# Kernel optimization log

Measured on AMD Instinct MI355X. Metric: run time of the kernel, lower is better.

The kernel has to match this reference:

```python
import jax, jax.numpy as jnp
import numpy as np

MODES = 16  # FourierLayer default


def _fourier_layer(h, w):
    # h: [B, S, H] real; w: [H, H, MODES] complex
    S = h.shape[1]
    h_ft = jnp.fft.rfft(h, axis=1)                 # [B, F, H] complex, F = S//2+1
    m = min(MODES, h_ft.shape[1])
    # batched complex matmul over the retained low-frequency modes
    out_m = jnp.einsum('bmh,hkm->bmk', h_ft[:, :m, :], w[:, :, :m])
    out_ft = jnp.zeros_like(h_ft).at[:, :m, :].set(out_m)  # higher modes zeroed
    h = jnp.fft.irfft(out_ft, n=S, axis=1)
    return jax.nn.gelu(h, approximate=False)       # torch nn.GELU() is exact erf


def setup_inputs() -> dict:
    key = jax.random.key(0)
    ks = jax.random.split(key, 7)
    B, S, H, L = 32, 8192, 128, 4
    x = jax.random.normal(ks[0], (B, S), jnp.float32)
    proj_w = jax.random.normal(ks[1], (H,), jnp.float32)          # Linear(1,H).weight[:,0]
    proj_b = jax.random.normal(ks[2], (H,), jnp.float32) * 0.02
    w_re = jax.random.normal(ks[3], (L, H, H, MODES), jnp.float32) * 0.02
    w_im = jax.random.normal(ks[4], (L, H, H, MODES), jnp.float32) * 0.02
    out_w = jax.random.normal(ks[5], (H,), jnp.float32) * 0.02    # Linear(H,1).weight[0]
    out_b = jax.random.normal(ks[6], (1,), jnp.float32) * 0.02
    return {"x": x, "proj_w": proj_w, "proj_b": proj_b,
            "w_re": w_re, "w_im": w_im, "out_w": out_w, "out_b": out_b}


def reference(x, proj_w, proj_b, w_re, w_im, out_w, out_b):
    # projection: Linear(1, H) applied to x.unsqueeze(-1)
    h = x[..., None] * proj_w + proj_b            # [B, S, H]
    W = (w_re + 1j * w_im).astype(jnp.complex64)  # [L, H, H, MODES]
    for l in range(w_re.shape[0]):                # fixed small layer count
        h = _fourier_layer(h, W[l])
    # output projection Linear(H, 1) then squeeze(-1)
    return h @ out_w + out_b[0]                   # [B, S]
```

## Files before the change

### kernel.cpp

```cpp
#include <hip/hip_runtime.h>
#include <hip/hip_bf16.h>

#define S_LEN 8192
#define NH 128
#define NM 16
#define NB 32
#define NBATCH 32
#define GP2 136

typedef __hip_bfloat16 bf16;
typedef unsigned short ushort_t;
typedef unsigned int uint_t;

typedef __bf16 bf16x8 __attribute__((ext_vector_type(8)));
typedef float floatx4 __attribute__((ext_vector_type(4)));

__device__ __forceinline__ float b2f(bf16 v){ return __bfloat162float(v); }
__device__ __forceinline__ float ldf(const void* p, long i, int f32){
    return f32 ? ((const float*)p)[i] : b2f(((const bf16*)p)[i]);
}
__device__ __forceinline__ float gelu_fast(float x){
    float z = fabsf(x) * 0.70710678118654752440f;
    float t = __builtin_amdgcn_rcpf(__builtin_fmaf(0.3275911f, z, 1.0f));
    float p = t*(0.254829592f + t*(-0.284496736f + t*(1.421413741f +
              t*(-1.453152027f + t*1.061405429f))));
    float e = __expf(-z * z);
    float er = __builtin_fmaf(-p, e, 1.0f);
    float s = copysignf(er, x);
    return 0.5f * x * (1.0f + s);
}
__device__ __forceinline__ ushort_t f2us(float v){
    return __builtin_bit_cast(ushort_t, (__bf16)v);
}
__device__ __forceinline__ void split_bf(float v, ushort_t& hi, ushort_t& lo){
    __bf16 h = (__bf16)v;
    float r = v - (float)h;
    hi = __builtin_bit_cast(ushort_t, h);
    lo = __builtin_bit_cast(ushort_t, (__bf16)r);
}
__device__ __forceinline__ bf16x8 ld8(const ushort_t* p){
    return *(const bf16x8*)(const void*)p;
}
__device__ __forceinline__ floatx4 MF(bf16x8 a, bf16x8 b, floatx4 c){
    return __builtin_amdgcn_mfma_f32_16x16x32_bf16(a, b, c, 0, 0, 0);
}

__device__ __forceinline__ int detect_f32(const void* x, int tid){
    __shared__ int sflag;
    if (tid < 64){
        const ushort_t* p = (const ushort_t*)x;
        int cnt = 0;
        for (int i = tid; i < 4096; i += 64){
            int e = (p[i] >> 7) & 0xFF;
            if (e >= 0xA0) cnt++;
        }
        #pragma unroll
        for (int off = 32; off > 0; off >>= 1) cnt += __shfl_xor(cnt, off, 64);
        if (tid == 0) sflag = (cnt > 400) ? 1 : 0;
    }
    __syncthreads();
    return sflag;
}

__device__ __forceinline__ void c_prologue(const float* __restrict__ C,
                                           int b, int c, int q,
                                           bf16x8* Bhi, bf16x8* Blo){
    const float* Cb = C + (long)b * NB * NH;
    #pragma unroll
    for (int kt = 0; kt < 8; kt++){
        int k = kt * 16 + c;
        bf16x8 h8, l8;
        #pragma unroll
        for (int e = 0; e < 8; e++){
            int j = 8 * q + e;
            float sc = (j == 0) ? (1.0f / S_LEN)
                     : (j < NM) ? (2.0f / S_LEN)
                     : (j == NM) ? 0.f : (-2.0f / S_LEN);
            float v = Cb[j * NH + k] * sc;
            __bf16 hh = (__bf16)v;
            h8[e] = hh;
            l8[e] = (__bf16)(v - (float)hh);
        }
        Bhi[kt] = h8; Blo[kt] = l8;
    }
}

__global__ __launch_bounds__(256) void k_prep(const void* __restrict__ x,
                                              const void* __restrict__ pw,
                                              const void* __restrict__ pb,
                                              float* __restrict__ M,
                                              ushort_t* __restrict__ Thi,
                                              ushort_t* __restrict__ Tlo,
                                              ushort_t* __restrict__ TThi,
                                              float* __restrict__ C0){
    int bid = blockIdx.x;
    int tid = threadIdx.x;
    int f32 = detect_f32(x, tid);
    if (bid < 512){
        int m = bid >> 5, b = bid & 31;
        float re = 0.f, im = 0.f;
        #pragma unroll 4
        for (int s = tid; s < S_LEN; s += 256){
            float xv = ldf(x, (long)b * S_LEN + s, f32);
            if (m){
                int r = (m * s) & (S_LEN - 1);
                float rev = (float)r * (1.0f / (float)S_LEN);
                float sv = __builtin_amdgcn_sinf(rev);
                float cv = __builtin_amdgcn_cosf(rev);
                re += xv * cv;
                im -= xv * sv;
            } else {
                re += xv;
            }
        }
        __shared__ float sred[8];
        #pragma unroll
        for (int off = 32; off > 0; off >>= 1){
            re += __shfl_xor(re, off, 64);
            im += __shfl_xor(im, off, 64);
        }
        int w = tid >> 6;
        if ((tid & 63) == 0){ sred[w] = re; sred[4 + w] = im; }
        __syncthreads();
        if (tid < NH){
            float Xre = sred[0] + sred[1] + sred[2] + sred[3];
            float Xim = sred[4] + sred[5] + sred[6] + sred[7];
            int h = tid;
            float pwv = ldf(pw, h, f32);
            float fc = pwv * Xre + (m == 0 ? (float)S_LEN * ldf(pb, h, f32) : 0.f);
            float fs = -pwv * Xim;
            float* Mb = M + (long)b * NB * NH;
            Mb[m * NH + h]        = fc;
            Mb[(NM + m) * NH + h] = fs;
        }
    } else {
        int bb = bid - 512;
        int s = bb * 16 + (tid >> 4);
        int m = tid & 15;
        float cv = 1.f, sv = 0.f;
        if (m){
            int r = (m * s) & (S_LEN - 1);
            float rev = (float)r * (1.0f / (float)S_LEN);
            sv = __builtin_amdgcn_sinf(rev);
            cv = __builtin_amdgcn_cosf(rev);
        }
        ushort_t chi, clo, shi, slo;
        split_bf(cv, chi, clo);
        split_bf(sv, shi, slo);
        Thi[s * NB + m] = chi;       Tlo[s * NB + m] = clo;
        Thi[s * NB + NM + m] = shi;  Tlo[s * NB + NM + m] = slo;
        TThi[m * S_LEN + s] = chi;
        TThi[(NM + m) * S_LEN + s] = shi;
        C0[bb * 256 + tid] = 0.f;
    }
}

__global__ __launch_bounds__(256) void k_mixA(const void* __restrict__ x,
                                              const float* __restrict__ Msrc,
                                              int nparts,
                                              const void* __restrict__ wre,
                                              const void* __restrict__ wim,
                                              long woff,
                                              float* __restrict__ C){
    int tid = threadIdx.x;
    int f32 = detect_f32(x, tid);
    int hc = blockIdx.x, b = blockIdx.y;
    int k = tid & 127, mh = tid >> 7;
    int m0 = mh * 8;
    int h0 = hc * 16;
    __shared__ float Ms[NB * 16];
    for (int i = tid; i < NB * 16; i += 256){
        int j = i >> 4, hh = i & 15;
        const float* mp = Msrc + (long)b * nparts * (NB * NH) + j * NH + h0 + hh;
        float acc = 0.f;
        for (int sx = 0; sx < nparts; sx++) acc += mp[(long)sx * NB * NH];
        Ms[j * 16 + hh] = acc;
    }
    __syncthreads();
    float Cr[8] = {0,0,0,0,0,0,0,0}, Ci[8] = {0,0,0,0,0,0,0,0};
    #pragma unroll 4
    for (int hh = 0; hh < 16; hh++){
        long base = woff + ((long)(h0 + hh) * NH + k) * NM + m0;
        float wr[8], wi[8];
        if (f32){
            const float4* wr4 = (const float4*)((const float*)wre + base);
            const float4* wi4 = (const float4*)((const float*)wim + base);
            float4 a0 = wr4[0], a1 = wr4[1], c0 = wi4[0], c1 = wi4[1];
            wr[0]=a0.x; wr[1]=a0.y; wr[2]=a0.z; wr[3]=a0.w;
            wr[4]=a1.x; wr[5]=a1.y; wr[6]=a1.z; wr[7]=a1.w;
            wi[0]=c0.x; wi[1]=c0.y; wi[2]=c0.z; wi[3]=c0.w;
            wi[4]=c1.x; wi[5]=c1.y; wi[6]=c1.z; wi[7]=c1.w;
        } else {
            bf16x8 a = ld8((const ushort_t*)wre + base);
            bf16x8 c = ld8((const ushort_t*)wim + base);
            #pragma unroll
            for (int e = 0; e < 8; e++){ wr[e] = (float)a[e]; wi[e] = (float)c[e]; }
        }
        #pragma unroll
        for (int e = 0; e < 8; e++){
            float fc = Ms[(m0 + e) * 16 + hh];
            float fs = Ms[(NM + m0 + e) * 16 + hh];
            Cr[e] += fc * wr[e] + fs * wi[e];
            Ci[e] += fc * wi[e] - fs * wr[e];
        }
    }
    float* Cb = C + (long)b * NB * NH;
    #pragma unroll
    for (int e = 0; e < 8; e++){
        atomicAdd(&Cb[(m0 + e) * NH + k],      Cr[e]);
        atomicAdd(&Cb[(NM + m0 + e) * NH + k], Ci[e]);
    }
}

__global__ __launch_bounds__(256, 4) void k_fused(const ushort_t* __restrict__ Thi,
                                                  const ushort_t* __restrict__ Tlo,
                                                  const ushort_t* __restrict__ TThi,
                                                  const float* __restrict__ C,
                                                  float* __restrict__ Cnext,
                                                  float* __restrict__ Mpart){
    int b = blockIdx.y;
    int sx = blockIdx.x;
    int s0 = sx * 256;
    int tid = threadIdx.x;
    int w = tid >> 6;
    int lane = tid & 63;
    int c = lane & 15, q = lane >> 4;
    __shared__ __align__(16) ushort_t Glds[NH * GP2];

    bf16x8 Bhi[8], Blo[8];
    c_prologue(C, b, c, q, Bhi, Blo);
    if (tid < 32){
        *(float4*)(Cnext + (long)b * NB * NH + sx * 128 + tid * 4)
            = (float4){0.f, 0.f, 0.f, 0.f};
    }
    floatx4 a00 = {0,0,0,0}, a01 = {0,0,0,0}, a10 = {0,0,0,0}, a11 = {0,0,0,0};
    int kt0 = 2 * w;
    for (int p = 0; p < 2; p++){
        int sp = s0 + p * 128;
        #pragma unroll
        for (int sti = 0; sti < 2; sti++){
            int st = w * 2 + sti;
            long ar = (long)(sp + st * 16 + c) * NB + 8 * q;
            bf16x8 Ahi = ld8(Thi + ar);
            bf16x8 Alo = ld8(Tlo + ar);
            #pragma unroll
            for (int kt = 0; kt < 8; kt++){
                floatx4 acc = {0.f, 0.f, 0.f, 0.f};
                acc = MF(Ahi, Bhi[kt], acc);
                acc = MF(Alo, Bhi[kt], acc);
                acc = MF(Ahi, Blo[kt], acc);
                uint_t u0 = (uint_t)f2us(gelu_fast(acc[0])) |
                            ((uint_t)f2us(gelu_fast(acc[1])) << 16);
                uint_t u1 = (uint_t)f2us(gelu_fast(acc[2])) |
                            ((uint_t)f2us(gelu_fast(acc[3])) << 16);
                uint_t* gp = (uint_t*)&Glds[(kt * 16 + c) * GP2 + st * 16 + 4 * q];
                gp[0] = u0; gp[1] = u1;
            }
        }
        __syncthreads();
        #pragma unroll
        for (int kk = 0; kk < 4; kk++){
            long sa = (long)sp + kk * 32 + 8 * q;
            bf16x8 A0h = ld8(TThi + (long)c * S_LEN + sa);
            bf16x8 A1h = ld8(TThi + (long)(16 + c) * S_LEN + sa);
            bf16x8 G0 = ld8(&Glds[(kt0 * 16 + c) * GP2 + kk * 32 + 8 * q]);
            bf16x8 G1 = ld8(&Glds[((kt0 + 1) * 16 + c) * GP2 + kk * 32 + 8 * q]);
            a00 = MF(A0h, G0, a00);
            a01 = MF(A0h, G1, a01);
            a10 = MF(A1h, G0, a10);
            a11 = MF(A1h, G1, a11);
        }
        __syncthreads();
    }
    float* Mb = Mpart + ((long)b * 32 + sx) * (NB * NH);
    #pragma unroll
    for (int r = 0; r < 4; r++){
        Mb[(4 * q + r) * NH + kt0 * 16 + c]            = a00[r];
        Mb[(4 * q + r) * NH + (kt0 + 1) * 16 + c]      = a01[r];
        Mb[(16 + 4 * q + r) * NH + kt0 * 16 + c]       = a10[r];
        Mb[(16 + 4 * q + r) * NH + (kt0 + 1) * 16 + c] = a11[r];
    }
}

__global__ __launch_bounds__(256) void k_final(const void* __restrict__ x,
                                               const ushort_t* __restrict__ Thi,
                                               const ushort_t* __restrict__ Tlo,
                                               const float* __restrict__ C,
                                               const void* __restrict__ ow,
                                               const void* __restrict__ ob,
                                               void* __restrict__ out){
    int tid = threadIdx.x;
    int f32 = detect_f32(x, tid);
    int b = blockIdx.y;
    int s0 = blockIdx.x * 128;
    int w = tid >> 6;
    int lane = tid & 63;
    int c = lane & 15, q = lane >> 4;

    bf16x8 Bhi[8], Blo[8];
    c_prologue(C, b, c, q, Bhi, Blo);
    float ow8[8];
    #pragma unroll
    for (int kt = 0; kt < 8; kt++) ow8[kt] = ldf(ow, kt * 16 + c, f32);
    float obv = ldf(ob, 0, f32);
    #pragma unroll
    for (int sti = 0; sti < 2; sti++){
        int st = w * 2 + sti;
        long ar = (long)(s0 + st * 16 + c) * NB + 8 * q;
        bf16x8 Ahi = ld8(Thi + ar);
        bf16x8 Alo = ld8(Tlo + ar);
        float p0 = 0.f, p1 = 0.f, p2 = 0.f, p3 = 0.f;
        #pragma unroll
        for (int g = 0; g < 2; g++){
            int k0 = g * 4;
            floatx4 ac[4];
            #pragma unroll
            for (int t = 0; t < 4; t++) ac[t] = (floatx4){0.f, 0.f, 0.f, 0.f};
            #pragma unroll
            for (int t = 0; t < 4; t++) ac[t] = MF(Ahi, Bhi[k0 + t], ac[t]);
            #pragma unroll
            for (int t = 0; t < 4; t++) ac[t] = MF(Alo, Bhi[k0 + t], ac[t]);
            #pragma unroll
            for (int t = 0; t < 4; t++) ac[t] = MF(Ahi, Blo[k0 + t], ac[t]);
            #pragma unroll
            for (int t = 0; t < 4; t++){
                float o = ow8[k0 + t];
                p0 += gelu_fast(ac[t][0]) * o;
                p1 += gelu_fast(ac[t][1]) * o;
                p2 += gelu_fast(ac[t][2]) * o;
                p3 += gelu_fast(ac[t][3]) * o;
            }
        }
        #pragma unroll
        for (int off = 1; off < 16; off <<= 1){
            p0 += __shfl_xor(p0, off, 16);
            p1 += __shfl_xor(p1, off, 16);
            p2 += __shfl_xor(p2, off, 16);
            p3 += __shfl_xor(p3, off, 16);
        }
        if (c == 0){
            long s = s0 + st * 16 + 4 * q;
            if (f32){
                float4 v = {p0 + obv, p1 + obv, p2 + obv, p3 + obv};
                *(float4*)((float*)out + (long)b * S_LEN + s) = v;
            } else {
                uint_t u0 = (uint_t)f2us(p0 + obv) | ((uint_t)f2us(p1 + obv) << 16);
                uint_t u1 = (uint_t)f2us(p2 + obv) | ((uint_t)f2us(p3 + obv) << 16);
                uint_t* gp = (uint_t*)((ushort_t*)out + (long)b * S_LEN + s);
                gp[0] = u0; gp[1] = u1;
            }
        }
    }
}

extern "C" void kernel_launch(void* const* d_in, const int* in_sizes, int n_in,
                              void* d_out, int out_size, void* d_ws, size_t ws_size,
                              hipStream_t stream) {
    const void* x   = d_in[0];
    const void* pw  = d_in[1];
    const void* pb  = d_in[2];
    const void* wre = d_in[3];
    const void* wim = d_in[4];
    const void* ow  = d_in[5];
    const void* ob  = d_in[6];

    char* ws = (char*)d_ws;
    ushort_t* Thi  = (ushort_t*)(ws);
    ushort_t* Tlo  = (ushort_t*)(ws + (512u << 10));
    ushort_t* TThi = (ushort_t*)(ws + (1024u << 10));
    float* C0    = (float*)(ws + (1536u << 10));
    float* C1    = (float*)(ws + (2048u << 10));
    float* Mfull = (float*)(ws + (2560u << 10));
    float* Mpart = (float*)(ws + (3072u << 10));

    const long wstride = (long)NH * NH * NM;

    k_prep<<<1024, 256, 0, stream>>>(x, pw, pb, Mfull, Thi, Tlo, TThi, C0);
    k_mixA<<<dim3(8, NBATCH), 256, 0, stream>>>(x, Mfull, 1, wre, wim,
                                                0 * wstride, C0);
    k_fused<<<dim3(32, NBATCH), 256, 0, stream>>>(Thi, Tlo, TThi, C0, C1, Mpart);
    k_mixA<<<dim3(8, NBATCH), 256, 0, stream>>>(x, Mpart, 32, wre, wim,
                                                1 * wstride, C1);
    k_fused<<<dim3(32, NBATCH), 256, 0, stream>>>(Thi, Tlo, TThi, C1, C0, Mpart);
    k_mixA<<<dim3(8, NBATCH), 256, 0, stream>>>(x, Mpart, 32, wre, wim,
                                                2 * wstride, C0);
    k_fused<<<dim3(32, NBATCH), 256, 0, stream>>>(Thi, Tlo, TThi, C0, C1, Mpart);
    k_mixA<<<dim3(8, NBATCH), 256, 0, stream>>>(x, Mpart, 32, wre, wim,
                                                3 * wstride, C1);
    k_final<<<dim3(64, NBATCH), 256, 0, stream>>>(x, Thi, Tlo, C1, ow, ob, d_out);
}
```

Before: 281.0 us.

## Restructure fused Fourier kernel to per-wave LDS tiles and separate partial reduction

```diff
diff --git a/kernel.cpp b/kernel.cpp
--- a/kernel.cpp
+++ b/kernel.cpp
@@ -6,7 +6,6 @@
 #define NM 16
 #define NB 32
 #define NBATCH 32
-#define GP2 136
 
 typedef __hip_bfloat16 bf16;
 typedef unsigned short ushort_t;
@@ -156,8 +155,7 @@
 }
 
 __global__ __launch_bounds__(256) void k_mixA(const void* __restrict__ x,
-                                              const float* __restrict__ Msrc,
-                                              int nparts,
+                                              const float* __restrict__ M,
                                               const void* __restrict__ wre,
                                               const void* __restrict__ wim,
                                               long woff,
@@ -171,10 +169,7 @@
     __shared__ float Ms[NB * 16];
     for (int i = tid; i < NB * 16; i += 256){
         int j = i >> 4, hh = i & 15;
-        const float* mp = Msrc + (long)b * nparts * (NB * NH) + j * NH + h0 + hh;
-        float acc = 0.f;
-        for (int sx = 0; sx < nparts; sx++) acc += mp[(long)sx * NB * NH];
-        Ms[j * 16 + hh] = acc;
+        Ms[j * 16 + hh] = M[(long)b * NB * NH + j * NH + h0 + hh];
     }
     __syncthreads();
     float Cr[8] = {0,0,0,0,0,0,0,0}, Ci[8] = {0,0,0,0,0,0,0,0};
@@ -212,65 +207,94 @@
     }
 }
 
-__global__ __launch_bounds__(256, 4) void k_fused(const ushort_t* __restrict__ Thi,
-                                                  const ushort_t* __restrict__ Tlo,
-                                                  const ushort_t* __restrict__ TThi,
-                                                  const float* __restrict__ C,
-                                                  float* __restrict__ Cnext,
-                                                  float* __restrict__ Mpart){
+__global__ __launch_bounds__(256) void k_reduce(const float* __restrict__ Mpart,
+                                                float* __restrict__ Mfull){
+    int r = blockIdx.x, b = blockIdx.y;
+    int idx = r * 256 + threadIdx.x;
+    const float* mp = Mpart + (long)b * 32 * (NB * NH) + idx;
+    float acc = 0.f;
+    #pragma unroll
+    for (int sx = 0; sx < 32; sx++) acc += mp[(long)sx * (NB * NH)];
+    Mfull[(long)b * (NB * NH) + idx] = acc;
+}
+
+__global__ __launch_bounds__(256, 4) void k_fused2(const ushort_t* __restrict__ Thi,
+                                                   const ushort_t* __restrict__ Tlo,
+                                                   const ushort_t* __restrict__ TThi,
+                                                   const float* __restrict__ C,
+                                                   float* __restrict__ Cnext,
+                                                   float* __restrict__ Mpart){
     int b = blockIdx.y;
     int sx = blockIdx.x;
-    int s0 = sx * 256;
     int tid = threadIdx.x;
     int w = tid >> 6;
     int lane = tid & 63;
     int c = lane & 15, q = lane >> 4;
-    __shared__ __align__(16) ushort_t Glds[NH * GP2];
-
-    bf16x8 Bhi[8], Blo[8];
-    c_prologue(C, b, c, q, Bhi, Blo);
+    int kt0 = 2 * w;
+    __shared__ __align__(16) ushort_t G[4][32][40];
+
+    bf16x8 Bhi[2], Blo[2];
+    {
+        const float* Cb = C + (long)b * NB * NH;
+        #pragma unroll
+        for (int ktl = 0; ktl < 2; ktl++){
+            int k = (kt0 + ktl) * 16 + c;
+            bf16x8 h8, l8;
+            #pragma unroll
+            for (int e = 0; e < 8; e++){
+                int j = 8 * q + e;
+                float sc = (j == 0) ? (1.0f / S_LEN)
+                         : (j < NM) ? (2.0f / S_LEN)
+                         : (j == NM) ? 0.f : (-2.0f / S_LEN);
+                float v = Cb[j * NH + k] * sc;
+                __bf16 hh = (__bf16)v;
+                h8[e] = hh;
+                l8[e] = (__bf16)(v - (float)hh);
+            }
+            Bhi[ktl] = h8; Blo[ktl] = l8;
+        }
+    }
     if (tid < 32){
         *(float4*)(Cnext + (long)b * NB * NH + sx * 128 + tid * 4)
             = (float4){0.f, 0.f, 0.f, 0.f};
     }
+
     floatx4 a00 = {0,0,0,0}, a01 = {0,0,0,0}, a10 = {0,0,0,0}, a11 = {0,0,0,0};
-    int kt0 = 2 * w;
-    for (int p = 0; p < 2; p++){
-        int sp = s0 + p * 128;
-        #pragma unroll
-        for (int sti = 0; sti < 2; sti++){
-            int st = w * 2 + sti;
-            long ar = (long)(sp + st * 16 + c) * NB + 8 * q;
-            bf16x8 Ahi = ld8(Thi + ar);
-            bf16x8 Alo = ld8(Tlo + ar);
-            #pragma unroll
-            for (int kt = 0; kt < 8; kt++){
+    int s0B = sx * 256;
+    #pragma unroll 2
+    for (int t2 = 0; t2 < 8; t2++){
+        int sc0 = s0B + 32 * t2;
+        bf16x8 Ahi[2], Alo[2];
+        #pragma unroll
+        for (int tt = 0; tt < 2; tt++){
+            long ar = (long)(sc0 + 16 * tt + c) * NB + 8 * q;
+            Ahi[tt] = ld8(Thi + ar);
+            Alo[tt] = ld8(Tlo + ar);
+        }
+        bf16x8 Att0 = ld8(TThi + (long)c * S_LEN + sc0 + 8 * q);
+        bf16x8 Att1 = ld8(TThi + (long)(16 + c) * S_LEN + sc0 + 8 * q);
+        #pragma unroll
+        for (int tt = 0; tt < 2; tt++){
+            #pragma unroll
+            for (int ktl = 0; ktl < 2; ktl++){
                 floatx4 acc = {0.f, 0.f, 0.f, 0.f};
-                acc = MF(Ahi, Bhi[kt], acc);
-                acc = MF(Alo, Bhi[kt], acc);
-                acc = MF(Ahi, Blo[kt], acc);
+                acc = MF(Ahi[tt], Bhi[ktl], acc);
+                acc = MF(Alo[tt], Bhi[ktl], acc);
+                acc = MF(Ahi[tt], Blo[ktl], acc);
                 uint_t u0 = (uint_t)f2us(gelu_fast(acc[0])) |
                             ((uint_t)f2us(gelu_fast(acc[1])) << 16);
                 uint_t u1 = (uint_t)f2us(gelu_fast(acc[2])) |
                             ((uint_t)f2us(gelu_fast(acc[3])) << 16);
-                uint_t* gp = (uint_t*)&Glds[(kt * 16 + c) * GP2 + st * 16 + 4 * q];
-                gp[0] = u0; gp[1] = u1;
+                uint2 uu; uu.x = u0; uu.y = u1;
+                *(uint2*)(void*)&G[w][16 * ktl + c][16 * tt + 4 * q] = uu;
             }
         }
-        __syncthreads();
-        #pragma unroll
-        for (int kk = 0; kk < 4; kk++){
-            long sa = (long)sp + kk * 32 + 8 * q;
-            bf16x8 A0h = ld8(TThi + (long)c * S_LEN + sa);
-            bf16x8 A1h = ld8(TThi + (long)(16 + c) * S_LEN + sa);
-            bf16x8 G0 = ld8(&Glds[(kt0 * 16 + c) * GP2 + kk * 32 + 8 * q]);
-            bf16x8 G1 = ld8(&Glds[((kt0 + 1) * 16 + c) * GP2 + kk * 32 + 8 * q]);
-            a00 = MF(A0h, G0, a00);
-            a01 = MF(A0h, G1, a01);
-            a10 = MF(A1h, G0, a10);
-            a11 = MF(A1h, G1, a11);
-        }
-        __syncthreads();
+        bf16x8 P0 = *(const bf16x8*)(const void*)&G[w][c][8 * q];
+        bf16x8 P1 = *(const bf16x8*)(const void*)&G[w][16 + c][8 * q];
+        a00 = MF(Att0, P0, a00);
+        a01 = MF(Att0, P1, a01);
+        a10 = MF(Att1, P0, a10);
+        a11 = MF(Att1, P1, a11);
     }
     float* Mb = Mpart + ((long)b * 32 + sx) * (NB * NH);
     #pragma unroll
@@ -376,16 +400,19 @@
     const long wstride = (long)NH * NH * NM;
 
     k_prep<<<1024, 256, 0, stream>>>(x, pw, pb, Mfull, Thi, Tlo, TThi, C0);
-    k_mixA<<<dim3(8, NBATCH), 256, 0, stream>>>(x, Mfull, 1, wre, wim,
+    k_mixA<<<dim3(8, NBATCH), 256, 0, stream>>>(x, Mfull, wre, wim,
                                                 0 * wstride, C0);
-    k_fused<<<dim3(32, NBATCH), 256, 0, stream>>>(Thi, Tlo, TThi, C0, C1, Mpart);
-    k_mixA<<<dim3(8, NBATCH), 256, 0, stream>>>(x, Mpart, 32, wre, wim,
+    k_fused2<<<dim3(32, NBATCH), 256, 0, stream>>>(Thi, Tlo, TThi, C0, C1, Mpart);
+    k_reduce<<<dim3(16, NBATCH), 256, 0, stream>>>(Mpart, Mfull);
+    k_mixA<<<dim3(8, NBATCH), 256, 0, stream>>>(x, Mfull, wre, wim,
                                                 1 * wstride, C1);
-    k_fused<<<dim3(32, NBATCH), 256, 0, stream>>>(Thi, Tlo, TThi, C1, C0, Mpart);
-    k_mixA<<<dim3(8, NBATCH), 256, 0, stream>>>(x, Mpart, 32, wre, wim,
+    k_fused2<<<dim3(32, NBATCH), 256, 0, stream>>>(Thi, Tlo, TThi, C1, C0, Mpart);
+    k_reduce<<<dim3(16, NBATCH), 256, 0, stream>>>(Mpart, Mfull);
+    k_mixA<<<dim3(8, NBATCH), 256, 0, stream>>>(x, Mfull, wre, wim,
                                                 2 * wstride, C0);
-    k_fused<<<dim3(32, NBATCH), 256, 0, stream>>>(Thi, Tlo, TThi, C0, C1, Mpart);
-    k_mixA<<<dim3(8, NBATCH), 256, 0, stream>>>(x, Mpart, 32, wre, wim,
+    k_fused2<<<dim3(32, NBATCH), 256, 0, stream>>>(Thi, Tlo, TThi, C0, C1, Mpart);
+    k_reduce<<<dim3(16, NBATCH), 256, 0, stream>>>(Mpart, Mfull);
+    k_mixA<<<dim3(8, NBATCH), 256, 0, stream>>>(x, Mfull, wre, wim,
                                                 3 * wstride, C1);
     k_final<<<dim3(64, NBATCH), 256, 0, stream>>>(x, Thi, Tlo, C1, ow, ob, d_out);
 }
```

After: 251.1 us. 10.7% less time.

## Split partial-sum reduction into its own kernel and widen mixA grid

Applied to the files above, without the earlier changes.

```diff
diff --git a/kernel.cpp b/kernel.cpp
--- a/kernel.cpp
+++ b/kernel.cpp
@@ -92,25 +92,40 @@
                                               ushort_t* __restrict__ Thi,
                                               ushort_t* __restrict__ Tlo,
                                               ushort_t* __restrict__ TThi,
-                                              float* __restrict__ C0){
+                                              float* __restrict__ C0,
+                                              uint_t* __restrict__ flag){
     int bid = blockIdx.x;
     int tid = threadIdx.x;
     int f32 = detect_f32(x, tid);
     if (bid < 512){
         int m = bid >> 5, b = bid & 31;
         float re = 0.f, im = 0.f;
-        #pragma unroll 4
-        for (int s = tid; s < S_LEN; s += 256){
-            float xv = ldf(x, (long)b * S_LEN + s, f32);
+        #pragma unroll
+        for (int g = 0; g < 4; g++){
+            int s0 = g * 2048 + tid * 8;
+            float xv[8];
+            if (f32){
+                const float4* xp = (const float4*)((const float*)x
+                                    + (long)b * S_LEN + s0);
+                float4 v0 = xp[0], v1 = xp[1];
+                xv[0]=v0.x; xv[1]=v0.y; xv[2]=v0.z; xv[3]=v0.w;
+                xv[4]=v1.x; xv[5]=v1.y; xv[6]=v1.z; xv[7]=v1.w;
+            } else {
+                bf16x8 v = ld8((const ushort_t*)x + (long)b * S_LEN + s0);
+                #pragma unroll
+                for (int e = 0; e < 8; e++) xv[e] = (float)v[e];
+            }
             if (m){
-                int r = (m * s) & (S_LEN - 1);
-                float rev = (float)r * (1.0f / (float)S_LEN);
-                float sv = __builtin_amdgcn_sinf(rev);
-                float cv = __builtin_amdgcn_cosf(rev);
-                re += xv * cv;
-                im -= xv * sv;
+                #pragma unroll
+                for (int e = 0; e < 8; e++){
+                    int r = (m * (s0 + e)) & (S_LEN - 1);
+                    float rev = (float)r * (1.0f / (float)S_LEN);
+                    re += xv[e] * __builtin_amdgcn_cosf(rev);
+                    im -= xv[e] * __builtin_amdgcn_sinf(rev);
+                }
             } else {
-                re += xv;
+                #pragma unroll
+                for (int e = 0; e < 8; e++) re += xv[e];
             }
         }
         __shared__ float sred[8];
@@ -152,52 +167,52 @@
         TThi[m * S_LEN + s] = chi;
         TThi[(NM + m) * S_LEN + s] = shi;
         C0[bb * 256 + tid] = 0.f;
-    }
-}
-
-__global__ __launch_bounds__(256) void k_mixA(const void* __restrict__ x,
-                                              const float* __restrict__ Msrc,
-                                              int nparts,
+        if (bb == 0 && tid == 0) flag[0] = (uint_t)f32;
+    }
+}
+
+__global__ __launch_bounds__(256) void k_mixA(const uint_t* __restrict__ flag,
+                                              const float* __restrict__ M,
                                               const void* __restrict__ wre,
                                               const void* __restrict__ wim,
                                               long woff,
                                               float* __restrict__ C){
     int tid = threadIdx.x;
-    int f32 = detect_f32(x, tid);
-    int hc = blockIdx.x, b = blockIdx.y;
-    int k = tid & 127, mh = tid >> 7;
-    int m0 = mh * 8;
+    int f32 = (int)flag[0];
+    int hc = blockIdx.x, mg = blockIdx.y, b = blockIdx.z;
+    int k = tid & 127, msub = tid >> 7;
+    int m0 = mg * 8 + msub * 4;
     int h0 = hc * 16;
     __shared__ float Ms[NB * 16];
     for (int i = tid; i < NB * 16; i += 256){
         int j = i >> 4, hh = i & 15;
-        const float* mp = Msrc + (long)b * nparts * (NB * NH) + j * NH + h0 + hh;
-        float acc = 0.f;
-        for (int sx = 0; sx < nparts; sx++) acc += mp[(long)sx * NB * NH];
-        Ms[j * 16 + hh] = acc;
+        Ms[j * 16 + hh] = M[(long)b * NB * NH + j * NH + h0 + hh];
     }
     __syncthreads();
-    float Cr[8] = {0,0,0,0,0,0,0,0}, Ci[8] = {0,0,0,0,0,0,0,0};
-    #pragma unroll 4
+    float Cr[4] = {0,0,0,0}, Ci[4] = {0,0,0,0};
+    #pragma unroll 8
     for (int hh = 0; hh < 16; hh++){
         long base = woff + ((long)(h0 + hh) * NH + k) * NM + m0;
-        float wr[8], wi[8];
+        float wr[4], wi[4];
         if (f32){
-            const float4* wr4 = (const float4*)((const float*)wre + base);
-            const float4* wi4 = (const float4*)((const float*)wim + base);
-            float4 a0 = wr4[0], a1 = wr4[1], c0 = wi4[0], c1 = wi4[1];
-            wr[0]=a0.x; wr[1]=a0.y; wr[2]=a0.z; wr[3]=a0.w;
-            wr[4]=a1.x; wr[5]=a1.y; wr[6]=a1.z; wr[7]=a1.w;
-            wi[0]=c0.x; wi[1]=c0.y; wi[2]=c0.z; wi[3]=c0.w;
-            wi[4]=c1.x; wi[5]=c1.y; wi[6]=c1.z; wi[7]=c1.w;
+            float4 a  = *(const float4*)((const float*)wre + base);
+            float4 cc = *(const float4*)((const float*)wim + base);
+            wr[0]=a.x;  wr[1]=a.y;  wr[2]=a.z;  wr[3]=a.w;
+            wi[0]=cc.x; wi[1]=cc.y; wi[2]=cc.z; wi[3]=cc.w;
         } else {
-            bf16x8 a = ld8((const ushort_t*)wre + base);
-            bf16x8 c = ld8((const ushort_t*)wim + base);
-            #pragma unroll
-            for (int e = 0; e < 8; e++){ wr[e] = (float)a[e]; wi[e] = (float)c[e]; }
-        }
-        #pragma unroll
-        for (int e = 0; e < 8; e++){
+            ushort4 a  = *(const ushort4*)((const ushort_t*)wre + base);
+            ushort4 cc = *(const ushort4*)((const ushort_t*)wim + base);
+            wr[0]=b2f(__builtin_bit_cast(bf16, a.x));
+            wr[1]=b2f(__builtin_bit_cast(bf16, a.y));
+            wr[2]=b2f(__builtin_bit_cast(bf16, a.z));
+            wr[3]=b2f(__builtin_bit_cast(bf16, a.w));
+            wi[0]=b2f(__builtin_bit_cast(bf16, cc.x));
+            wi[1]=b2f(__builtin_bit_cast(bf16, cc.y));
+            wi[2]=b2f(__builtin_bit_cast(bf16, cc.z));
+            wi[3]=b2f(__builtin_bit_cast(bf16, cc.w));
+        }
+        #pragma unroll
+        for (int e = 0; e < 4; e++){
             float fc = Ms[(m0 + e) * 16 + hh];
             float fs = Ms[(NM + m0 + e) * 16 + hh];
             Cr[e] += fc * wr[e] + fs * wi[e];
@@ -206,10 +221,21 @@
     }
     float* Cb = C + (long)b * NB * NH;
     #pragma unroll
-    for (int e = 0; e < 8; e++){
+    for (int e = 0; e < 4; e++){
         atomicAdd(&Cb[(m0 + e) * NH + k],      Cr[e]);
         atomicAdd(&Cb[(NM + m0 + e) * NH + k], Ci[e]);
     }
+}
+
+__global__ __launch_bounds__(256) void k_reduce(const float* __restrict__ Mpart,
+                                                float* __restrict__ Mfull){
+    int r = blockIdx.x, b = blockIdx.y;
+    int idx = r * 256 + threadIdx.x;
+    const float* mp = Mpart + (long)b * 32 * (NB * NH) + idx;
+    float acc = 0.f;
+    #pragma unroll
+    for (int sx = 0; sx < 32; sx++) acc += mp[(long)sx * (NB * NH)];
+    Mfull[(long)b * (NB * NH) + idx] = acc;
 }
 
 __global__ __launch_bounds__(256, 4) void k_fused(const ushort_t* __restrict__ Thi,
@@ -282,7 +308,7 @@
     }
 }
 
-__global__ __launch_bounds__(256) void k_final(const void* __restrict__ x,
+__global__ __launch_bounds__(256) void k_final(const uint_t* __restrict__ flag,
                                                const ushort_t* __restrict__ Thi,
                                                const ushort_t* __restrict__ Tlo,
                                                const float* __restrict__ C,
@@ -290,7 +316,7 @@
                                                const void* __restrict__ ob,
                                                void* __restrict__ out){
     int tid = threadIdx.x;
-    int f32 = detect_f32(x, tid);
+    int f32 = (int)flag[0];
     int b = blockIdx.y;
     int s0 = blockIdx.x * 128;
     int w = tid >> 6;
@@ -371,21 +397,26 @@
     float* C0    = (float*)(ws + (1536u << 10));
     float* C1    = (float*)(ws + (2048u << 10));
     float* Mfull = (float*)(ws + (2560u << 10));
-    float* Mpart = (float*)(ws + (3072u << 10));
+    uint_t* flag = (uint_t*)(ws + (3072u << 10));
+    float* Mpart = (float*)(ws + (3136u << 10));
 
     const long wstride = (long)NH * NH * NM;
 
-    k_prep<<<1024, 256, 0, stream>>>(x, pw, pb, Mfull, Thi, Tlo, TThi, C0);
-    k_mixA<<<dim3(8, NBATCH), 256, 0, stream>>>(x, Mfull, 1, wre, wim,
-                                                0 * wstride, C0);
+    k_prep<<<1024, 256, 0, stream>>>(x, pw, pb, Mfull, Thi, Tlo, TThi, C0, flag);
+    k_mixA<<<dim3(8, 2, NBATCH), 256, 0, stream>>>(flag, Mfull, wre, wim,
+                                                   0 * wstride, C0);
     k_fused<<<dim3(32, NBATCH), 256, 0, stream>>>(Thi, Tlo, TThi, C0, C1, Mpart);
-    k_mixA<<<dim3(8, NBATCH), 256, 0, stream>>>(x, Mpart, 32, wre, wim,
-                                                1 * wstride, C1);
+    k_reduce<<<dim3(16, NBATCH), 256, 0, stream>>>(Mpart, Mfull);
+    k_mixA<<<dim3(8, 2, NBATCH), 256, 0, stream>>>(flag, Mfull, wre, wim,
+                                                   1 * wstride, C1);
     k_fused<<<dim3(32, NBATCH), 256, 0, stream>>>(Thi, Tlo, TThi, C1, C0, Mpart);
-    k_mixA<<<dim3(8, NBATCH), 256, 0, stream>>>(x, Mpart, 32, wre, wim,
-                                                2 * wstride, C0);
+    k_reduce<<<dim3(16, NBATCH), 256, 0, stream>>>(Mpart, Mfull);
+    k_mixA<<<dim3(8, 2, NBATCH), 256, 0, stream>>>(flag, Mfull, wre, wim,
+                                                   2 * wstride, C0);
     k_fused<<<dim3(32, NBATCH), 256, 0, stream>>>(Thi, Tlo, TThi, C0, C1, Mpart);
-    k_mixA<<<dim3(8, NBATCH), 256, 0, stream>>>(x, Mpart, 32, wre, wim,
-                                                3 * wstride, C1);
-    k_final<<<dim3(64, NBATCH), 256, 0, stream>>>(x, Thi, Tlo, C1, ow, ob, d_out);
-}
+    k_reduce<<<dim3(16, NBATCH), 256, 0, stream>>>(Mpart, Mfull);
+    k_mixA<<<dim3(8, 2, NBATCH), 256, 0, stream>>>(flag, Mfull, wre, wim,
+                                                   3 * wstride, C1);
+    k_final<<<dim3(64, NBATCH), 256, 0, stream>>>(flag, Thi, Tlo, C1,
+                                                  ow, ob, d_out);
+}
```

Measured after the change: 245.0 us. 12.8% less time.
